# Optimization experiments

Hardware: AMD Instinct MI355X
Metric: run time of the kernel (lower is better)

The kernel has to match this reference:

```python
import jax, jax.numpy as jnp
import numpy as np
from jax import lax

B, S, T = 32, 100, 4
NUM_C2, NUM_C3, NUM_D, DV = 500, 2000, 1000, 128


def setup_inputs():
    key = jax.random.key(0)
    ks = jax.random.split(key, 25)
    s = 0.05
    def nrm(k, shape):
        return jax.random.normal(k, shape, dtype=jnp.float32) * s
    return {
        "c2_seq": jax.random.randint(ks[0], (B, S), 0, NUM_C2),
        "c3_seq": jax.random.randint(ks[1], (B, S, T), 1, NUM_C3 + 1),  # 0 is padding; use all-valid tags
        "d_seq": jax.random.randint(ks[2], (B, S), 0, NUM_D),
        "r_seq": jax.random.randint(ks[3], (B, S), 0, 2),
        "D_emb": nrm(ks[4], (NUM_D, 1)),
        "R_emb": nrm(ks[5], (2, DV)),
        "v_c2": nrm(ks[6], (DV,)),
        "v_c3": nrm(ks[7], (DV,)),
        "v_d": nrm(ks[8], (DV,)),
        "W_ih": nrm(ks[9], (3 * DV, 2 * DV)),
        "W_hh": nrm(ks[10], (3 * DV, DV)),
        "b_ih": nrm(ks[11], (3 * DV,)),
        "b_hh": nrm(ks[12], (3 * DV,)),
        "l1_W1": nrm(ks[13], (DV, DV)), "l1_b1": nrm(ks[14], (DV,)),
        "l1_W2": nrm(ks[15], (1, DV)), "l1_b2": nrm(ks[16], (1,)),
        "l2_W1": nrm(ks[17], (DV, 4 * DV)), "l2_b1": nrm(ks[18], (DV,)),
        "l2_W2": nrm(ks[19], (1, DV)), "l2_b2": nrm(ks[20], (1,)),
        "l3_W1": nrm(ks[21], (DV, 4 * DV)), "l3_b1": nrm(ks[22], (DV,)),
        "l3_W2": nrm(ks[23], (1, DV)), "l3_b2": nrm(ks[24], (1,)),
    }


def _mlp(x, W1, b1, W2, b2):
    # Linear -> ReLU -> (Dropout: identity in eval) -> Linear -> (Dropout)
    return jnp.maximum(x @ W1.T + b1, 0.0) @ W2.T + b2


def _gru(x_seq, h0, W_ih, W_hh, b_ih, b_hh):
    # torch.nn.GRU math, batch_first
    def step(h, x):
        gi = x @ W_ih.T + b_ih
        gh = h @ W_hh.T + b_hh
        i_r, i_z, i_n = jnp.split(gi, 3, axis=-1)
        h_r, h_z, h_n = jnp.split(gh, 3, axis=-1)
        r = jax.nn.sigmoid(i_r + h_r)
        z = jax.nn.sigmoid(i_z + h_z)
        n = jnp.tanh(i_n + r * h_n)
        h_new = (1.0 - z) * n + z * h
        return h_new, h_new
    _, hs = lax.scan(step, h0, jnp.swapaxes(x_seq, 0, 1))
    return jnp.swapaxes(hs, 0, 1)


def _forward(c2_seq, c3_seq, d_seq, r_seq, p):
    (D_emb, R_emb, v_c2, v_c3, v_d, W_ih, W_hh, b_ih, b_hh,
     l1_W1, l1_b1, l1_W2, l1_b2, l2_W1, l2_b1, l2_W2, l2_b2,
     l3_W1, l3_b1, l3_W2, l3_b2) = p
    Bn = c2_seq.shape[0]
    gamma = D_emb[d_seq]                      # [B,S,1]
    v_d_seq = gamma * v_d                     # [B,S,DV]
    v_r_seq = R_emb[r_seq]                    # [B,S,DV]
    h0 = jnp.zeros((Bn, DV), dtype=v_d_seq.dtype)
    h_seq = _gru(jnp.concatenate([v_d_seq, v_r_seq], -1), h0, W_ih, W_hh, b_ih, b_hh)
    alpha_seq = _mlp(h_seq, l1_W1, l1_b1, l1_W2, l1_b2)[..., 0]   # [B,S]

    def step(carry, xs):
        C2, C3 = carry
        c2, c3, vd, vr = xs                                      # [B],[B,T],[B,DV],[B,DV]
        mask = (c3 != 0).astype(C3.dtype)                        # [B,T]
        w = mask / mask.sum(-1, keepdims=True)
        beta2 = jnp.take_along_axis(C2, c2[:, None], axis=-1)    # [B,1]
        beta3 = jnp.take_along_axis(C3, c3, axis=-1)             # [B,T]
        beta3_bar = (beta3 * w).sum(-1)                          # [B]
        vc2 = beta2 * v_c2                                       # [B,DV]
        vc3 = beta3[..., None] * v_c3                            # [B,T,DV]
        vc3_bar = beta3_bar[:, None] * v_c3                      # [B,DV]
        new_c2 = _mlp(jnp.concatenate([vc2, vc3_bar, vd, vr], -1),
                      l2_W1, l2_b1, l2_W2, l2_b2)[:, 0]          # [B]
        feat3 = jnp.concatenate([
            jnp.broadcast_to(vc2[:, None, :], vc3.shape), vc3,
            jnp.broadcast_to(vd[:, None, :], vc3.shape),
            jnp.broadcast_to(vr[:, None, :], vc3.shape)], -1)    # [B,T,4*DV]
        new_c3 = _mlp(feat3, l3_W1, l3_b1, l3_W2, l3_b2)[..., 0]  # [B,T]
        oh2 = jax.nn.one_hot(c2, NUM_C2, dtype=C2.dtype)          # [B,NC2]
        oh3 = jax.nn.one_hot(c3, NUM_C3 + 1, dtype=C3.dtype) * mask[..., None]  # [B,T,NC3+1]
        multi = oh3.sum(1)
        C2n = C2 * (1.0 - oh2) + new_c2[:, None] * oh2
        C3n = C3 * (1.0 - multi) + (new_c3[..., None] * oh3).sum(1)
        return (C2n, C3n), (C2n, C3n)

    C2_0 = jnp.zeros((Bn, NUM_C2), dtype=jnp.float32)
    C3_0 = jnp.zeros((Bn, NUM_C3 + 1), dtype=jnp.float32)
    xs = (jnp.swapaxes(c2_seq, 0, 1), jnp.swapaxes(c3_seq, 0, 1),
          jnp.swapaxes(v_d_seq, 0, 1), jnp.swapaxes(v_r_seq, 0, 1))
    _, (C2_seq, C3_seq) = lax.scan(step, (C2_0, C3_0), xs)
    C2_seq = jnp.swapaxes(C2_seq, 0, 1)   # [B,S,NUM_C2]
    C3_seq = jnp.swapaxes(C3_seq, 0, 1)   # [B,S,NUM_C3+1]
    return alpha_seq, h_seq, C2_seq, C3_seq


def reference(c2_seq, c3_seq, d_seq, r_seq, D_emb, R_emb, v_c2, v_c3, v_d,
              W_ih, W_hh, b_ih, b_hh, l1_W1, l1_b1, l1_W2, l1_b2,
              l2_W1, l2_b1, l2_W2, l2_b2, l3_W1, l3_b1, l3_W2, l3_b2):
    p = (D_emb, R_emb, v_c2, v_c3, v_d, W_ih, W_hh, b_ih, b_hh,
         l1_W1, l1_b1, l1_W2, l1_b2, l2_W1, l2_b1, l2_W2, l2_b2,
         l3_W1, l3_b1, l3_W2, l3_b2)
    return _forward(c2_seq, c3_seq, d_seq, r_seq, p)
```

## Files before the change

kernel.cpp:

```cpp
#include <hip/hip_runtime.h>

#define BB   32
#define SS   100
#define TT   4
#define NCC2 500
#define NC3P 2001
#define DD   128

#define LDSF 14680

typedef _Float16 half2v __attribute__((ext_vector_type(2)));

#if defined(__has_builtin)
#if __has_builtin(__builtin_amdgcn_fdot2)
#define HAVE_FDOT2 1
#endif
#endif

__device__ __forceinline__ float fast_rcp(float x) { return __builtin_amdgcn_rcpf(x); }

__device__ __forceinline__ float dpp_sum64(float x) {
    x += __int_as_float(__builtin_amdgcn_update_dpp(0, __float_as_int(x), 0x111, 0xf, 0xf, true));
    x += __int_as_float(__builtin_amdgcn_update_dpp(0, __float_as_int(x), 0x112, 0xf, 0xf, true));
    x += __int_as_float(__builtin_amdgcn_update_dpp(0, __float_as_int(x), 0x114, 0xf, 0xf, true));
    x += __int_as_float(__builtin_amdgcn_update_dpp(0, __float_as_int(x), 0x118, 0xf, 0xf, true));
    x += __int_as_float(__builtin_amdgcn_update_dpp(0, __float_as_int(x), 0x142, 0xa, 0xf, true));
    x += __int_as_float(__builtin_amdgcn_update_dpp(0, __float_as_int(x), 0x143, 0xc, 0xf, true));
    return x;
}

__device__ __forceinline__ float dpp_sum16(float x) {
    x += __int_as_float(__builtin_amdgcn_update_dpp(0, __float_as_int(x), 0x111, 0xf, 0xf, true));
    x += __int_as_float(__builtin_amdgcn_update_dpp(0, __float_as_int(x), 0x112, 0xf, 0xf, true));
    x += __int_as_float(__builtin_amdgcn_update_dpp(0, __float_as_int(x), 0x114, 0xf, 0xf, true));
    x += __int_as_float(__builtin_amdgcn_update_dpp(0, __float_as_int(x), 0x118, 0xf, 0xf, true));
    return x;
}

__device__ __forceinline__ float dot4(float4 a, float4 b) {
    return fmaf(a.x, b.x, fmaf(a.y, b.y, fmaf(a.z, b.z, a.w * b.w)));
}

__device__ __forceinline__ unsigned pk16(float a, float b) {
    return __builtin_bit_cast(unsigned, __builtin_amdgcn_cvt_pkrtz(a, b));
}
__device__ __forceinline__ uint4 packf16(float4 A, float4 B) {
    uint4 u;
    u.x = pk16(A.x, A.y); u.y = pk16(A.z, A.w);
    u.z = pk16(B.x, B.y); u.w = pk16(B.z, B.w);
    return u;
}

__device__ __forceinline__ float dot2acc(unsigned w, unsigned h, float acc) {
#ifdef HAVE_FDOT2
    return __builtin_amdgcn_fdot2(__builtin_bit_cast(half2v, w),
                                  __builtin_bit_cast(half2v, h), acc, false);
#else
    half2v a = __builtin_bit_cast(half2v, w), b = __builtin_bit_cast(half2v, h);
    acc = fmaf((float)a.x, (float)b.x, acc);
    return fmaf((float)a.y, (float)b.y, acc);
#endif
}

__global__ __launch_bounds__(768, 1) void k_main(
    const int* __restrict__ c2_seq, const int* __restrict__ c3_seq,
    const int* __restrict__ d_seq,  const int* __restrict__ r_seq,
    const float* __restrict__ D_emb, const float* __restrict__ Remb,
    const float* __restrict__ v_c2, const float* __restrict__ v_c3,
    const float* __restrict__ v_d,
    const float* __restrict__ W_ih, const float* __restrict__ W_hh,
    const float* __restrict__ b_ih, const float* __restrict__ b_hh,
    const float* __restrict__ l2W1, const float* __restrict__ l2b1,
    const float* __restrict__ l2W2, const float* __restrict__ l2b2,
    const float* __restrict__ l3W1, const float* __restrict__ l3b1,
    const float* __restrict__ l3W2, const float* __restrict__ l3b2,
    float* __restrict__ h_out, float* __restrict__ C2o, float* __restrict__ C3o)
{
    __shared__ __align__(16) float sh[LDSF];
    int* shi = (int*)sh;
    const int blk = blockIdx.x;
    const int t = threadIdx.x;

    if (blk < BB) {
        const int b  = blk;
        const int w  = t >> 6, l = t & 63;
        const int p4 = w & 3;
        const int j2 = (w >> 2) * 64 + l;
        const int jA = j2, jB = j2 + 192;
        const int kb = p4 * 32;

        uint4 wa0, wa1, wa2, wa3, wb0, wb1, wb2, wb3;
        {
            const float4* ra = (const float4*)(W_hh + jA * DD + kb);
            const float4* rb = (const float4*)(W_hh + jB * DD + kb);
            wa0 = packf16(ra[0], ra[1]); wa1 = packf16(ra[2], ra[3]);
            wa2 = packf16(ra[4], ra[5]); wa3 = packf16(ra[6], ra[7]);
            wb0 = packf16(rb[0], rb[1]); wb1 = packf16(rb[2], rb[3]);
            wb2 = packf16(rb[4], rb[5]); wb3 = packf16(rb[6], rb[7]);
        }

        {
            const float4* vd4 = (const float4*)(v_d + kb);
            const float4* r04 = (const float4*)(Remb + kb);
            const float4* r14 = (const float4*)(Remb + 128 + kb);
#pragma unroll
            for (int rr2 = 0; rr2 < 2; ++rr2) {
                const int j = rr2 ? jB : jA;
                const float4* wx = (const float4*)(W_ih + j * 256 + kb);
                const float4* wr = (const float4*)(W_ih + j * 256 + 128 + kb);
                float pd = 0.f, pr0 = 0.f, pr1 = 0.f;
#pragma unroll
                for (int i = 0; i < 8; ++i) {
                    float4 a = wx[i], c = wr[i];
                    float4 vd = vd4[i], r0 = r04[i], r1 = r14[i];
                    pd  = fmaf(a.x, vd.x, fmaf(a.y, vd.y, fmaf(a.z, vd.z, fmaf(a.w, vd.w, pd))));
                    pr0 = fmaf(c.x, r0.x, fmaf(c.y, r0.y, fmaf(c.z, r0.z, fmaf(c.w, r0.w, pr0))));
                    pr1 = fmaf(c.x, r1.x, fmaf(c.y, r1.y, fmaf(c.z, r1.z, fmaf(c.w, r1.w, pr1))));
                }
                sh[1880 + p4 * 388 + j] = pd;
                sh[3432 + p4 * 388 + j] = pr0;
                sh[4984 + p4 * 388 + j] = pr1;
            }
        }
        if (t < SS) {
            sh[1680 + t]  = D_emb[d_seq[b * SS + t]];
            shi[1780 + t] = r_seq[b * SS + t];
        }
        if (t < 64) ((unsigned*)sh)[t] = 0u;
        __syncthreads();

        float gd_r=0,gd_z=0,gd_n=0, g0_r=0,g0_z=0,g0_n=0, g1_r=0,g1_z=0,g1_n=0;
        float bi_r=0,bi_z=0,bi_n=0, bh_r=0,bh_z=0,bh_n=0, h = 0.f;
        if (t < DD) {
#pragma unroll
            for (int p = 0; p < 4; ++p) {
                gd_r += sh[1880 + p * 388 + t];
                gd_z += sh[1880 + p * 388 + 128 + t];
                gd_n += sh[1880 + p * 388 + 256 + t];
                g0_r += sh[3432 + p * 388 + t];
                g0_z += sh[3432 + p * 388 + 128 + t];
                g0_n += sh[3432 + p * 388 + 256 + t];
                g1_r += sh[4984 + p * 388 + t];
                g1_z += sh[4984 + p * 388 + 128 + t];
                g1_n += sh[4984 + p * 388 + 256 + t];
            }
            bi_r = b_ih[t]; bi_z = b_ih[t+128]; bi_n = b_ih[t+256];
            bh_r = b_hh[t]; bh_z = b_hh[t+128]; bh_n = b_hh[t+256];
        }
        __syncthreads();

        for (int s = 0; s < SS; ++s) {
            float aA = 0.f, aB = 0.f;
            {
                const uint4* hb = ((const uint4*)sh) + p4 * 4;
                uint4 h0 = hb[0], h1 = hb[1], h2 = hb[2], h3 = hb[3];
                aA = dot2acc(wa0.x, h0.x, aA); aA = dot2acc(wa0.y, h0.y, aA);
                aA = dot2acc(wa0.z, h0.z, aA); aA = dot2acc(wa0.w, h0.w, aA);
                aA = dot2acc(wa1.x, h1.x, aA); aA = dot2acc(wa1.y, h1.y, aA);
                aA = dot2acc(wa1.z, h1.z, aA); aA = dot2acc(wa1.w, h1.w, aA);
                aA = dot2acc(wa2.x, h2.x, aA); aA = dot2acc(wa2.y, h2.y, aA);
                aA = dot2acc(wa2.z, h2.z, aA); aA = dot2acc(wa2.w, h2.w, aA);
                aA = dot2acc(wa3.x, h3.x, aA); aA = dot2acc(wa3.y, h3.y, aA);
                aA = dot2acc(wa3.z, h3.z, aA); aA = dot2acc(wa3.w, h3.w, aA);
                aB = dot2acc(wb0.x, h0.x, aB); aB = dot2acc(wb0.y, h0.y, aB);
                aB = dot2acc(wb0.z, h0.z, aB); aB = dot2acc(wb0.w, h0.w, aB);
                aB = dot2acc(wb1.x, h1.x, aB); aB = dot2acc(wb1.y, h1.y, aB);
                aB = dot2acc(wb1.z, h1.z, aB); aB = dot2acc(wb1.w, h1.w, aB);
                aB = dot2acc(wb2.x, h2.x, aB); aB = dot2acc(wb2.y, h2.y, aB);
                aB = dot2acc(wb2.z, h2.z, aB); aB = dot2acc(wb2.w, h2.w, aB);
                aB = dot2acc(wb3.x, h3.x, aB); aB = dot2acc(wb3.y, h3.y, aB);
                aB = dot2acc(wb3.z, h3.z, aB); aB = dot2acc(wb3.w, h3.w, aB);
            }
            sh[128 + p4 * 388 + jA] = aA;
            sh[128 + p4 * 388 + jB] = aB;
            __syncthreads();
            if (t < DD) {
                float ghr = bh_r, ghz = bh_z, ghn = bh_n;
#pragma unroll
                for (int p = 0; p < 4; ++p) {
                    ghr += sh[128 + p * 388 + t];
                    ghz += sh[128 + p * 388 + 128 + t];
                    ghn += sh[128 + p * 388 + 256 + t];
                }
                float gamma = sh[1680 + s]; int rr = shi[1780 + s];
                float gir = fmaf(gamma, gd_r, (rr ? g1_r : g0_r) + bi_r);
                float giz = fmaf(gamma, gd_z, (rr ? g1_z : g0_z) + bi_z);
                float gin = fmaf(gamma, gd_n, (rr ? g1_n : g0_n) + bi_n);
                float r = fast_rcp(1.f + __expf(-(gir + ghr)));
                float z = fast_rcp(1.f + __expf(-(giz + ghz)));
                float n = 1.f - 2.f * fast_rcp(__expf(2.f * fmaf(r, ghn, gin)) + 1.f);
                h = (1.f - z) * n + z * h;
                ((_Float16*)sh)[t] = (_Float16)h;
                sh[1880 + s * DD + t] = h;
            }
            __syncthreads();
        }

        {
            const float4* hs = (const float4*)(sh + 1880);
            float4* hd = (float4*)(h_out + (size_t)b * SS * DD);
            for (int i = t; i < SS * DD / 4; i += 768) hd[i] = hs[i];
        }
    } else {
        const int sb = blk - BB;
        const int b = sb >> 2;
        const int q = sb & 3;

        {
            const int g = (t & 63) >> 4, c8 = ((t & 63) & 15) * 8;
            const float* vsrc = (g == 0) ? v_c2 : (g == 1) ? v_c3 : (g == 2) ? v_d : Remb;
            const float4 va  = *(const float4*)(vsrc + c8);
            const float4 vb  = *(const float4*)(vsrc + c8 + 4);
            const float4 va1 = *(const float4*)(Remb + 128 + c8);
            const float4 vb1 = *(const float4*)(Remb + 132 + c8);
            for (int r = t >> 6; r < 256; r += 12) {
                const float* W = (r < 128) ? l2W1 : l3W1;
                float* U = sh + ((r < 128) ? 3264 : 3904);
                const int i = r & 127;
                const float* wr = W + i * 512 + g * 128 + c8;
                const float4 w0 = *(const float4*)(wr);
                const float4 w1 = *(const float4*)(wr + 4);
                float p  = dot4(w0, va)  + dot4(w1, vb);
                float p1 = dot4(w0, va1) + dot4(w1, vb1);
                p  = dpp_sum16(p);
                p1 = dpp_sum16(p1);
                if ((t & 15) == 15) {
                    U[g * 128 + i] = p;
                    if (g == 3) U[512 + i] = p1;
                }
            }
        }
        for (int k = t; k < NCC2 + NC3P; k += 768) sh[k] = 0.f;
        for (int k = t; k < SS; k += 768) {
            shi[2504 + k] = c2_seq[b * SS + k];
            sh[3004 + k]  = D_emb[d_seq[b * SS + k]];
            shi[3104 + k] = r_seq[b * SS + k];
        }
        for (int k = t; k < SS; k += 768)
            reinterpret_cast<int4*>(shi + 2604)[k] = reinterpret_cast<const int4*>(c3_seq + b * SS * TT)[k];
        __syncthreads();

        if (t < 64) {
            float* C2s = sh;
            float* C3s = sh + NCC2;
            const float* u2 = sh + 3264;
            const float* u3 = sh + 3904;
            const float u2a0 = u2[t],        u2a1 = u2[64 + t];
            const float u2b0 = u2[128 + t],  u2b1 = u2[192 + t];
            const float u2c0 = u2[256 + t],  u2c1 = u2[320 + t];
            const float u2d00 = u2[384 + t], u2d01 = u2[448 + t];
            const float u2d10 = u2[512 + t], u2d11 = u2[576 + t];
            const float u3a0 = u3[t],        u3a1 = u3[64 + t];
            const float u3b0 = u3[128 + t],  u3b1 = u3[192 + t];
            const float u3c0 = u3[256 + t],  u3c1 = u3[320 + t];
            const float u3d00 = u3[384 + t], u3d01 = u3[448 + t];
            const float u3d10 = u3[512 + t], u3d11 = u3[576 + t];
            const float b2_0 = l2b1[t], b2_1 = l2b1[64 + t];
            const float w2_0 = l2W2[t], w2_1 = l2W2[64 + t];
            const float b3_0 = l3b1[t], b3_1 = l3b1[64 + t];
            const float w3_0 = l3W2[t], w3_1 = l3W2[64 + t];
            const float c2bias = l2b2[0], c3bias = l3b2[0];

            int  nc2 = shi[2504];
            int4 nc3 = reinterpret_cast<const int4*>(shi + 2604)[0];
            float ngam = sh[3004];
            int   nrr  = shi[3104];

            for (int s = 0; s < SS; ++s) {
                const int c2i = nc2;
                const int i0 = nc3.x, i1 = nc3.y, i2 = nc3.z, i3 = nc3.w;
                const float gamma = ngam;
                const int rr = nrr;
                if (s + 1 < SS) {
                    nc2 = shi[2504 + s + 1];
                    nc3 = reinterpret_cast<const int4*>(shi + 2604)[s + 1];
                    ngam = sh[3004 + s + 1];
                    nrr  = shi[3104 + s + 1];
                }

                const float beta2 = C2s[c2i];
                const bool k0 = (i0 != 0), k1 = (i1 != 0), k2 = (i2 != 0), k3 = (i3 != 0);
                const float m0 = k0 ? 1.f : 0.f, m1 = k1 ? 1.f : 0.f;
                const float m2 = k2 ? 1.f : 0.f, m3 = k3 ? 1.f : 0.f;
                const float bt0 = C3s[i0], bt1 = C3s[i1], bt2 = C3s[i2], bt3 = C3s[i3];
                const float msum = m0 + m1 + m2 + m3;
                const float b3bar = (bt0 * m0 + bt1 * m1 + bt2 * m2 + bt3 * m3) * fast_rcp(msum);

                const float ud20 = rr ? u2d10 : u2d00, ud21 = rr ? u2d11 : u2d01;
                const float ud30 = rr ? u3d10 : u3d00, ud31 = rr ? u3d11 : u3d01;

                float h20 = fmaf(beta2, u2a0, fmaf(b3bar, u2b0, fmaf(gamma, u2c0, ud20 + b2_0)));
                float h21 = fmaf(beta2, u2a1, fmaf(b3bar, u2b1, fmaf(gamma, u2c1, ud21 + b2_1)));
                float newc2 = dpp_sum64(fmaf(fmaxf(h20, 0.f), w2_0, fmaxf(h21, 0.f) * w2_1)) + c2bias;

                const float base30 = fmaf(beta2, u3a0, fmaf(gamma, u3c0, ud30 + b3_0));
                const float base31 = fmaf(beta2, u3a1, fmaf(gamma, u3c1, ud31 + b3_1));
                float ha, hb, q0, q1, q2, q3;
                ha = fmaf(bt0, u3b0, base30); hb = fmaf(bt0, u3b1, base31);
                q0 = dpp_sum64(fmaf(fmaxf(ha, 0.f), w3_0, fmaxf(hb, 0.f) * w3_1)) + c3bias;
                ha = fmaf(bt1, u3b0, base30); hb = fmaf(bt1, u3b1, base31);
                q1 = dpp_sum64(fmaf(fmaxf(ha, 0.f), w3_0, fmaxf(hb, 0.f) * w3_1)) + c3bias;
                ha = fmaf(bt2, u3b0, base30); hb = fmaf(bt2, u3b1, base31);
                q2 = dpp_sum64(fmaf(fmaxf(ha, 0.f), w3_0, fmaxf(hb, 0.f) * w3_1)) + c3bias;
                ha = fmaf(bt3, u3b0, base30); hb = fmaf(bt3, u3b1, base31);
                q3 = dpp_sum64(fmaf(fmaxf(ha, 0.f), w3_0, fmaxf(hb, 0.f) * w3_1)) + c3bias;

                float val0, val1, val2, val3;
                {
                    float c = m0 + ((k1 && i1 == i0) ? 1.f : 0.f) + ((k2 && i2 == i0) ? 1.f : 0.f) + ((k3 && i3 == i0) ? 1.f : 0.f);
                    float qs = (k0 ? q0 : 0.f) + ((k1 && i1 == i0) ? q1 : 0.f) + ((k2 && i2 == i0) ? q2 : 0.f) + ((k3 && i3 == i0) ? q3 : 0.f);
                    val0 = bt0 * (1.f - c) + qs;
                }
                {
                    float c = ((k0 && i0 == i1) ? 1.f : 0.f) + m1 + ((k2 && i2 == i1) ? 1.f : 0.f) + ((k3 && i3 == i1) ? 1.f : 0.f);
                    float qs = ((k0 && i0 == i1) ? q0 : 0.f) + (k1 ? q1 : 0.f) + ((k2 && i2 == i1) ? q2 : 0.f) + ((k3 && i3 == i1) ? q3 : 0.f);
                    val1 = bt1 * (1.f - c) + qs;
                }
                {
                    float c = ((k0 && i0 == i2) ? 1.f : 0.f) + ((k1 && i1 == i2) ? 1.f : 0.f) + m2 + ((k3 && i3 == i2) ? 1.f : 0.f);
                    float qs = ((k0 && i0 == i2) ? q0 : 0.f) + ((k1 && i1 == i2) ? q1 : 0.f) + (k2 ? q2 : 0.f) + ((k3 && i3 == i2) ? q3 : 0.f);
                    val2 = bt2 * (1.f - c) + qs;
                }
                {
                    float c = ((k0 && i0 == i3) ? 1.f : 0.f) + ((k1 && i1 == i3) ? 1.f : 0.f) + ((k2 && i2 == i3) ? 1.f : 0.f) + m3;
                    float qs = ((k0 && i0 == i3) ? q0 : 0.f) + ((k1 && i1 == i3) ? q1 : 0.f) + ((k2 && i2 == i3) ? q2 : 0.f) + (k3 ? q3 : 0.f);
                    val3 = bt3 * (1.f - c) + qs;
                }

                if (t == 63) {
                    C2s[c2i] = newc2;
                    if (k0) C3s[i0] = val0;
                    if (k1) C3s[i1] = val1;
                    if (k2) C3s[i2] = val2;
                    if (k3) C3s[i3] = val3;
                    sh[4544 + s] = newc2;
                    sh[4644 + 4 * s + 0] = val0;
                    sh[4644 + 4 * s + 1] = val1;
                    sh[4644 + 4 * s + 2] = val2;
                    sh[4644 + 4 * s + 3] = val3;
                }
            }
        }
        __syncthreads();

        for (int k = t; k < NCC2 + NC3P; k += 768) sh[k] = 0.f;
        __syncthreads();

        float* C2s = sh;
        float* C3s = sh + NCC2;
        for (int s = 0; s < SS; ++s) {
            if (t == 0) {
                C2s[shi[2504 + s]] = sh[4544 + s];
                const int4 ic3 = reinterpret_cast<const int4*>(shi + 2604)[s];
                if (ic3.x) C3s[ic3.x] = sh[4644 + 4 * s + 0];
                if (ic3.y) C3s[ic3.y] = sh[4644 + 4 * s + 1];
                if (ic3.z) C3s[ic3.z] = sh[4644 + 4 * s + 2];
                if (ic3.w) C3s[ic3.w] = sh[4644 + 4 * s + 3];
            }
            if ((s & 3) == q) {
                __syncthreads();
                const int rs = b * SS + s;
                float* c2row = C2o + (size_t)rs * NCC2;
                if (t < 125) reinterpret_cast<float4*>(c2row)[t] = reinterpret_cast<const float4*>(C2s)[t];
                float* c3row = C3o + (size_t)rs * NC3P;
                const int p0 = (4 - (rs & 3)) & 3;
                if (t < p0) c3row[t] = C3s[t];
                const int rem = NC3P - p0;
                const int nv = rem >> 2, tl = rem & 3;
                if (t < nv) {
                    const int d = p0 + 4 * t;
                    *reinterpret_cast<float4*>(c3row + d) =
                        make_float4(C3s[d], C3s[d + 1], C3s[d + 2], C3s[d + 3]);
                }
                if (t < tl) {
                    const int d = p0 + 4 * nv + t;
                    c3row[d] = C3s[d];
                }
                __syncthreads();
            }
        }
    }
}

__global__ __launch_bounds__(256) void k_alpha(const float* __restrict__ h_seq,
                                               const float* __restrict__ W1,
                                               const float* __restrict__ b1,
                                               const float* __restrict__ W2,
                                               const float* __restrict__ b2,
                                               float* __restrict__ alpha)
{
    __shared__ __align__(16) float sl[22560];
    const int t = threadIdx.x;
    const int base = blockIdx.x * 16;

    float4* hl4 = reinterpret_cast<float4*>(sl);
    const float4* hg = reinterpret_cast<const float4*>(h_seq + (size_t)base * DD);
    for (int i = t; i < 512; i += 256) hl4[i] = hg[i];

    float4* wl4 = reinterpret_cast<float4*>(sl + 6144);
    const float4* wg = reinterpret_cast<const float4*>(W1);
    for (int g = t; g < 4096; g += 256) {
        const int ch = g >> 5, k4 = g & 31;
        wl4[ch * 32 + (k4 ^ (ch & 31))] = wg[g];
    }
    __syncthreads();

    const int ch = t & 127, half = t >> 7;
    float acc[16];
#pragma unroll
    for (int r = 0; r < 16; ++r) acc[r] = 0.f;
#pragma unroll
    for (int kk = 0; kk < 16; ++kk) {
        const int k4 = half * 16 + kk;
        const float4 w = wl4[ch * 32 + (k4 ^ (ch & 31))];
#pragma unroll
        for (int r = 0; r < 16; ++r) {
            const float4 hv = hl4[r * 32 + k4];
            acc[r] = fmaf(w.x, hv.x, fmaf(w.y, hv.y, fmaf(w.z, hv.z, fmaf(w.w, hv.w, acc[r]))));
        }
    }
#pragma unroll
    for (int r = 0; r < 16; ++r) sl[2048 + r * 256 + t] = acc[r];
    __syncthreads();
    if (t < 128) {
        const float b1v = b1[t], w2v = W2[t];
#pragma unroll
        for (int r = 0; r < 16; ++r) {
            float v = fmaxf(sl[2048 + r * 256 + t] + sl[2048 + r * 256 + 128 + t] + b1v, 0.f) * w2v;
            v = dpp_sum64(v);
            if ((t & 63) == 63) sl[22528 + r * 2 + (t >> 6)] = v;
        }
    }
    __syncthreads();
    if (t < 16) alpha[base + t] = sl[22528 + 2 * t] + sl[22528 + 2 * t + 1] + b2[0];
}

extern "C" void kernel_launch(void* const* d_in, const int* in_sizes, int n_in,
                              void* d_out, int out_size, void* d_ws, size_t ws_size,
                              hipStream_t stream)
{
    (void)in_sizes; (void)n_in; (void)out_size; (void)d_ws; (void)ws_size;
    const int*   c2_seq = (const int*)d_in[0];
    const int*   c3_seq = (const int*)d_in[1];
    const int*   d_seq  = (const int*)d_in[2];
    const int*   r_seq  = (const int*)d_in[3];
    const float* D_emb  = (const float*)d_in[4];
    const float* Remb   = (const float*)d_in[5];
    const float* v_c2   = (const float*)d_in[6];
    const float* v_c3   = (const float*)d_in[7];
    const float* v_d    = (const float*)d_in[8];
    const float* W_ih   = (const float*)d_in[9];
    const float* W_hh   = (const float*)d_in[10];
    const float* b_ih   = (const float*)d_in[11];
    const float* b_hh   = (const float*)d_in[12];
    const float* l1W1   = (const float*)d_in[13];
    const float* l1b1   = (const float*)d_in[14];
    const float* l1W2   = (const float*)d_in[15];
    const float* l1b2   = (const float*)d_in[16];
    const float* l2W1   = (const float*)d_in[17];
    const float* l2b1   = (const float*)d_in[18];
    const float* l2W2   = (const float*)d_in[19];
    const float* l2b2   = (const float*)d_in[20];
    const float* l3W1   = (const float*)d_in[21];
    const float* l3b1   = (const float*)d_in[22];
    const float* l3W2   = (const float*)d_in[23];
    const float* l3b2   = (const float*)d_in[24];

    float* out   = (float*)d_out;
    float* alpha = out;
    float* h_out = out + 3200;
    float* C2o   = out + 412800;
    float* C3o   = out + 2012800;

    k_main<<<BB + 4 * BB, 768, 0, stream>>>(c2_seq, c3_seq, d_seq, r_seq, D_emb, Remb,
                                            v_c2, v_c3, v_d,
                                            W_ih, W_hh, b_ih, b_hh,
                                            l2W1, l2b1, l2W2, l2b2,
                                            l3W1, l3b1, l3W2, l3b2,
                                            h_out, C2o, C3o);
    k_alpha<<<200, 256, 0, stream>>>(h_out, l1W1, l1b1, l1W2, l1b2, alpha);
}
```

Before: 118.4 us.

## Fuse alpha MLP into main kernel, shrink blocks to 512, rework C-state pipeline

```diff
diff --git a/kernel.cpp b/kernel.cpp
--- a/kernel.cpp
+++ b/kernel.cpp
@@ -7,7 +7,14 @@
 #define NC3P 2001
 #define DD   128
 
-#define LDSF 14680
+#define ALPH  0
+#define REDB  2048
+#define GAMB  2064
+#define RRB   2164
+#define HALL  2264
+#define PARTB 15064
+#define HF16  16632
+#define LDSF  16696
 
 typedef _Float16 half2v __attribute__((ext_vector_type(2)));
 
@@ -35,6 +42,10 @@
     x += __int_as_float(__builtin_amdgcn_update_dpp(0, __float_as_int(x), 0x114, 0xf, 0xf, true));
     x += __int_as_float(__builtin_amdgcn_update_dpp(0, __float_as_int(x), 0x118, 0xf, 0xf, true));
     return x;
+}
+
+__device__ __forceinline__ float rdl63(float x) {
+    return __int_as_float(__builtin_amdgcn_readlane(__float_as_int(x), 63));
 }
 
 __device__ __forceinline__ float dot4(float4 a, float4 b) {
@@ -62,7 +73,18 @@
 #endif
 }
 
-__global__ __launch_bounds__(768, 1) void k_main(
+#define DOTQ(w0, w1, w2, w3, h0, h1, h2, h3, acc) do {                     \
+    acc = dot2acc((w0).x, (h0).x, acc); acc = dot2acc((w0).y, (h0).y, acc);\
+    acc = dot2acc((w0).z, (h0).z, acc); acc = dot2acc((w0).w, (h0).w, acc);\
+    acc = dot2acc((w1).x, (h1).x, acc); acc = dot2acc((w1).y, (h1).y, acc);\
+    acc = dot2acc((w1).z, (h1).z, acc); acc = dot2acc((w1).w, (h1).w, acc);\
+    acc = dot2acc((w2).x, (h2).x, acc); acc = dot2acc((w2).y, (h2).y, acc);\
+    acc = dot2acc((w2).z, (h2).z, acc); acc = dot2acc((w2).w, (h2).w, acc);\
+    acc = dot2acc((w3).x, (h3).x, acc); acc = dot2acc((w3).y, (h3).y, acc);\
+    acc = dot2acc((w3).z, (h3).z, acc); acc = dot2acc((w3).w, (h3).w, acc);\
+} while (0)
+
+__global__ __launch_bounds__(512, 1) void k_all(
     const int* __restrict__ c2_seq, const int* __restrict__ c3_seq,
     const int* __restrict__ d_seq,  const int* __restrict__ r_seq,
     const float* __restrict__ D_emb, const float* __restrict__ Remb,
@@ -70,33 +92,39 @@
     const float* __restrict__ v_d,
     const float* __restrict__ W_ih, const float* __restrict__ W_hh,
     const float* __restrict__ b_ih, const float* __restrict__ b_hh,
+    const float* __restrict__ l1W1, const float* __restrict__ l1b1,
+    const float* __restrict__ l1W2, const float* __restrict__ l1b2,
     const float* __restrict__ l2W1, const float* __restrict__ l2b1,
     const float* __restrict__ l2W2, const float* __restrict__ l2b2,
     const float* __restrict__ l3W1, const float* __restrict__ l3b1,
     const float* __restrict__ l3W2, const float* __restrict__ l3b2,
-    float* __restrict__ h_out, float* __restrict__ C2o, float* __restrict__ C3o)
+    float* __restrict__ alpha, float* __restrict__ h_out,
+    float* __restrict__ C2o, float* __restrict__ C3o)
 {
     __shared__ __align__(16) float sh[LDSF];
     int* shi = (int*)sh;
+    float4* sh4 = (float4*)sh;
     const int blk = blockIdx.x;
     const int t = threadIdx.x;
 
     if (blk < BB) {
-        const int b  = blk;
-        const int w  = t >> 6, l = t & 63;
-        const int p4 = w & 3;
-        const int j2 = (w >> 2) * 64 + l;
-        const int jA = j2, jB = j2 + 192;
+        const int b = blk;
+        const int trip = t >> 2;
+        const int p4 = t & 3;
+        const int jA = 3 * trip, jB = jA + 1, jC = jA + 2;
         const int kb = p4 * 32;
 
-        uint4 wa0, wa1, wa2, wa3, wb0, wb1, wb2, wb3;
+        uint4 wa0, wa1, wa2, wa3, wb0, wb1, wb2, wb3, wc0, wc1, wc2, wc3;
         {
             const float4* ra = (const float4*)(W_hh + jA * DD + kb);
             const float4* rb = (const float4*)(W_hh + jB * DD + kb);
+            const float4* rc = (const float4*)(W_hh + jC * DD + kb);
             wa0 = packf16(ra[0], ra[1]); wa1 = packf16(ra[2], ra[3]);
             wa2 = packf16(ra[4], ra[5]); wa3 = packf16(ra[6], ra[7]);
             wb0 = packf16(rb[0], rb[1]); wb1 = packf16(rb[2], rb[3]);
             wb2 = packf16(rb[4], rb[5]); wb3 = packf16(rb[6], rb[7]);
+            wc0 = packf16(rc[0], rc[1]); wc1 = packf16(rc[2], rc[3]);
+            wc2 = packf16(rc[4], rc[5]); wc3 = packf16(rc[6], rc[7]);
         }
 
         {
@@ -104,8 +132,8 @@
             const float4* r04 = (const float4*)(Remb + kb);
             const float4* r14 = (const float4*)(Remb + 128 + kb);
 #pragma unroll
-            for (int rr2 = 0; rr2 < 2; ++rr2) {
-                const int j = rr2 ? jB : jA;
+            for (int rr3 = 0; rr3 < 3; ++rr3) {
+                const int j = jA + rr3;
                 const float4* wx = (const float4*)(W_ih + j * 256 + kb);
                 const float4* wr = (const float4*)(W_ih + j * 256 + 128 + kb);
                 float pd = 0.f, pr0 = 0.f, pr1 = 0.f;
@@ -117,16 +145,16 @@
                     pr0 = fmaf(c.x, r0.x, fmaf(c.y, r0.y, fmaf(c.z, r0.z, fmaf(c.w, r0.w, pr0))));
                     pr1 = fmaf(c.x, r1.x, fmaf(c.y, r1.y, fmaf(c.z, r1.z, fmaf(c.w, r1.w, pr1))));
                 }
-                sh[1880 + p4 * 388 + j] = pd;
-                sh[3432 + p4 * 388 + j] = pr0;
-                sh[4984 + p4 * 388 + j] = pr1;
+                sh[HALL +        p4 * 392 + j] = pd;
+                sh[HALL + 1568 + p4 * 392 + j] = pr0;
+                sh[HALL + 3136 + p4 * 392 + j] = pr1;
             }
         }
         if (t < SS) {
-            sh[1680 + t]  = D_emb[d_seq[b * SS + t]];
-            shi[1780 + t] = r_seq[b * SS + t];
-        }
-        if (t < 64) ((unsigned*)sh)[t] = 0u;
+            sh[GAMB + t]  = D_emb[d_seq[b * SS + t]];
+            shi[RRB + t] = r_seq[b * SS + t];
+        }
+        if (t < 64) ((unsigned*)(sh + HF16))[t] = 0u;
         __syncthreads();
 
         float gd_r=0,gd_z=0,gd_n=0, g0_r=0,g0_z=0,g0_n=0, g1_r=0,g1_z=0,g1_n=0;
@@ -134,15 +162,15 @@
         if (t < DD) {
 #pragma unroll
             for (int p = 0; p < 4; ++p) {
-                gd_r += sh[1880 + p * 388 + t];
-                gd_z += sh[1880 + p * 388 + 128 + t];
-                gd_n += sh[1880 + p * 388 + 256 + t];
-                g0_r += sh[3432 + p * 388 + t];
-                g0_z += sh[3432 + p * 388 + 128 + t];
-                g0_n += sh[3432 + p * 388 + 256 + t];
-                g1_r += sh[4984 + p * 388 + t];
-                g1_z += sh[4984 + p * 388 + 128 + t];
-                g1_n += sh[4984 + p * 388 + 256 + t];
+                gd_r += sh[HALL + p * 392 + t];
+                gd_z += sh[HALL + p * 392 + 128 + t];
+                gd_n += sh[HALL + p * 392 + 256 + t];
+                g0_r += sh[HALL + 1568 + p * 392 + t];
+                g0_z += sh[HALL + 1568 + p * 392 + 128 + t];
+                g0_n += sh[HALL + 1568 + p * 392 + 256 + t];
+                g1_r += sh[HALL + 3136 + p * 392 + t];
+                g1_z += sh[HALL + 3136 + p * 392 + 128 + t];
+                g1_n += sh[HALL + 3136 + p * 392 + 256 + t];
             }
             bi_r = b_ih[t]; bi_z = b_ih[t+128]; bi_n = b_ih[t+256];
             bh_r = b_hh[t]; bh_z = b_hh[t+128]; bh_n = b_hh[t+256];
@@ -150,39 +178,27 @@
         __syncthreads();
 
         for (int s = 0; s < SS; ++s) {
-            float aA = 0.f, aB = 0.f;
+            float aA = 0.f, aB = 0.f, aC = 0.f;
             {
-                const uint4* hb = ((const uint4*)sh) + p4 * 4;
+                const uint4* hb = ((const uint4*)(sh + HF16)) + p4 * 4;
                 uint4 h0 = hb[0], h1 = hb[1], h2 = hb[2], h3 = hb[3];
-                aA = dot2acc(wa0.x, h0.x, aA); aA = dot2acc(wa0.y, h0.y, aA);
-                aA = dot2acc(wa0.z, h0.z, aA); aA = dot2acc(wa0.w, h0.w, aA);
-                aA = dot2acc(wa1.x, h1.x, aA); aA = dot2acc(wa1.y, h1.y, aA);
-                aA = dot2acc(wa1.z, h1.z, aA); aA = dot2acc(wa1.w, h1.w, aA);
-                aA = dot2acc(wa2.x, h2.x, aA); aA = dot2acc(wa2.y, h2.y, aA);
-                aA = dot2acc(wa2.z, h2.z, aA); aA = dot2acc(wa2.w, h2.w, aA);
-                aA = dot2acc(wa3.x, h3.x, aA); aA = dot2acc(wa3.y, h3.y, aA);
-                aA = dot2acc(wa3.z, h3.z, aA); aA = dot2acc(wa3.w, h3.w, aA);
-                aB = dot2acc(wb0.x, h0.x, aB); aB = dot2acc(wb0.y, h0.y, aB);
-                aB = dot2acc(wb0.z, h0.z, aB); aB = dot2acc(wb0.w, h0.w, aB);
-                aB = dot2acc(wb1.x, h1.x, aB); aB = dot2acc(wb1.y, h1.y, aB);
-                aB = dot2acc(wb1.z, h1.z, aB); aB = dot2acc(wb1.w, h1.w, aB);
-                aB = dot2acc(wb2.x, h2.x, aB); aB = dot2acc(wb2.y, h2.y, aB);
-                aB = dot2acc(wb2.z, h2.z, aB); aB = dot2acc(wb2.w, h2.w, aB);
-                aB = dot2acc(wb3.x, h3.x, aB); aB = dot2acc(wb3.y, h3.y, aB);
-                aB = dot2acc(wb3.z, h3.z, aB); aB = dot2acc(wb3.w, h3.w, aB);
-            }
-            sh[128 + p4 * 388 + jA] = aA;
-            sh[128 + p4 * 388 + jB] = aB;
+                DOTQ(wa0, wa1, wa2, wa3, h0, h1, h2, h3, aA);
+                DOTQ(wb0, wb1, wb2, wb3, h0, h1, h2, h3, aB);
+                DOTQ(wc0, wc1, wc2, wc3, h0, h1, h2, h3, aC);
+            }
+            sh[PARTB + p4 * 392 + jA] = aA;
+            sh[PARTB + p4 * 392 + jB] = aB;
+            sh[PARTB + p4 * 392 + jC] = aC;
             __syncthreads();
             if (t < DD) {
                 float ghr = bh_r, ghz = bh_z, ghn = bh_n;
 #pragma unroll
                 for (int p = 0; p < 4; ++p) {
-                    ghr += sh[128 + p * 388 + t];
-                    ghz += sh[128 + p * 388 + 128 + t];
-                    ghn += sh[128 + p * 388 + 256 + t];
-                }
-                float gamma = sh[1680 + s]; int rr = shi[1780 + s];
+                    ghr += sh[PARTB + p * 392 + t];
+                    ghz += sh[PARTB + p * 392 + 128 + t];
+                    ghn += sh[PARTB + p * 392 + 256 + t];
+                }
+                float gamma = sh[GAMB + s]; int rr = shi[RRB + s];
                 float gir = fmaf(gamma, gd_r, (rr ? g1_r : g0_r) + bi_r);
                 float giz = fmaf(gamma, gd_z, (rr ? g1_z : g0_z) + bi_z);
                 float gin = fmaf(gamma, gd_n, (rr ? g1_n : g0_n) + bi_n);
@@ -190,21 +206,62 @@
                 float z = fast_rcp(1.f + __expf(-(giz + ghz)));
                 float n = 1.f - 2.f * fast_rcp(__expf(2.f * fmaf(r, ghn, gin)) + 1.f);
                 h = (1.f - z) * n + z * h;
-                ((_Float16*)sh)[t] = (_Float16)h;
-                sh[1880 + s * DD + t] = h;
+                ((_Float16*)(sh + HF16))[t] = (_Float16)h;
+                sh[HALL + s * DD + t] = h;
             }
             __syncthreads();
         }
 
         {
-            const float4* hs = (const float4*)(sh + 1880);
+            const float4* hs = (const float4*)(sh + HALL);
             float4* hd = (float4*)(h_out + (size_t)b * SS * DD);
-            for (int i = t; i < SS * DD / 4; i += 768) hd[i] = hs[i];
+            for (int i = t; i < SS * DD / 4; i += 512) hd[i] = hs[i];
+        }
+
+        {
+            const int ch = t & 127, seg = t >> 7;
+            float4 aw[8];
+            const float4* awp = (const float4*)(l1W1 + ch * 128 + seg * 32);
+#pragma unroll
+            for (int i = 0; i < 8; ++i) aw[i] = awp[i];
+            float b1v = 0.f, w2v = 0.f;
+            if (t < 128) { b1v = l1b1[t]; w2v = l1W2[t]; }
+            const float b2v = l1b2[0];
+
+            for (int r0 = 0; r0 < SS; r0 += 4) {
+                float acc0 = 0.f, acc1 = 0.f, acc2 = 0.f, acc3 = 0.f;
+                const int hbase = (HALL >> 2) + seg * 8;
+#pragma unroll
+                for (int i = 0; i < 8; ++i) {
+                    acc0 = fmaf(1.f, dot4(aw[i], sh4[hbase + (r0 + 0) * 32 + i]), acc0);
+                    acc1 = fmaf(1.f, dot4(aw[i], sh4[hbase + (r0 + 1) * 32 + i]), acc1);
+                    acc2 = fmaf(1.f, dot4(aw[i], sh4[hbase + (r0 + 2) * 32 + i]), acc2);
+                    acc3 = fmaf(1.f, dot4(aw[i], sh4[hbase + (r0 + 3) * 32 + i]), acc3);
+                }
+                sh[ALPH + 0 * 512 + seg * 128 + ch] = acc0;
+                sh[ALPH + 1 * 512 + seg * 128 + ch] = acc1;
+                sh[ALPH + 2 * 512 + seg * 128 + ch] = acc2;
+                sh[ALPH + 3 * 512 + seg * 128 + ch] = acc3;
+                __syncthreads();
+                if (t < 128) {
+#pragma unroll
+                    for (int rr4 = 0; rr4 < 4; ++rr4) {
+                        float v = sh[ALPH + rr4 * 512 + t] + sh[ALPH + rr4 * 512 + 128 + t]
+                                + sh[ALPH + rr4 * 512 + 256 + t] + sh[ALPH + rr4 * 512 + 384 + t];
+                        v = fmaxf(v + b1v, 0.f) * w2v;
+                        v = dpp_sum64(v);
+                        if ((t & 63) == 63) sh[REDB + rr4 * 2 + (t >> 6)] = v;
+                    }
+                }
+                __syncthreads();
+                if (t < 4) alpha[b * SS + r0 + t] = sh[REDB + 2 * t] + sh[REDB + 2 * t + 1] + b2v;
+                __syncthreads();
+            }
         }
     } else {
         const int sb = blk - BB;
-        const int b = sb >> 2;
-        const int q = sb & 3;
+        const int b = sb >> 3;
+        const int q = sb & 7;
 
         {
             const int g = (t & 63) >> 4, c8 = ((t & 63) & 15) * 8;
@@ -213,7 +270,7 @@
             const float4 vb  = *(const float4*)(vsrc + c8 + 4);
             const float4 va1 = *(const float4*)(Remb + 128 + c8);
             const float4 vb1 = *(const float4*)(Remb + 132 + c8);
-            for (int r = t >> 6; r < 256; r += 12) {
+            for (int r = t >> 6; r < 256; r += 8) {
                 const float* W = (r < 128) ? l2W1 : l3W1;
                 float* U = sh + ((r < 128) ? 3264 : 3904);
                 const int i = r & 127;
@@ -230,13 +287,13 @@
                 }
             }
         }
-        for (int k = t; k < NCC2 + NC3P; k += 768) sh[k] = 0.f;
-        for (int k = t; k < SS; k += 768) {
+        for (int k = t; k < NCC2 + NC3P; k += 512) sh[k] = 0.f;
+        for (int k = t; k < SS; k += 512) {
             shi[2504 + k] = c2_seq[b * SS + k];
             sh[3004 + k]  = D_emb[d_seq[b * SS + k]];
             shi[3104 + k] = r_seq[b * SS + k];
         }
-        for (int k = t; k < SS; k += 768)
+        for (int k = t; k < SS; k += 512)
             reinterpret_cast<int4*>(shi + 2604)[k] = reinterpret_cast<const int4*>(c3_seq + b * SS * TT)[k];
         __syncthreads();
 
@@ -261,89 +318,98 @@
             const float w3_0 = l3W2[t], w3_1 = l3W2[64 + t];
             const float c2bias = l2b2[0], c3bias = l3b2[0];
 
-            int  nc2 = shi[2504];
-            int4 nc3 = reinterpret_cast<const int4*>(shi + 2604)[0];
-            float ngam = sh[3004];
-            int   nrr  = shi[3104];
+            float beta2 = 0.f, bt0 = 0.f, bt1 = 0.f, bt2 = 0.f, bt3 = 0.f;
+            int c2i = shi[2504];
+            int4 i4 = reinterpret_cast<const int4*>(shi + 2604)[0];
+            float gamma = sh[3004];
+            int   rr    = shi[3104];
 
             for (int s = 0; s < SS; ++s) {
-                const int c2i = nc2;
-                const int i0 = nc3.x, i1 = nc3.y, i2 = nc3.z, i3 = nc3.w;
-                const float gamma = ngam;
-                const int rr = nrr;
+                int nc2i = 0; int4 ni4 = make_int4(0, 0, 0, 0);
+                float ngam = 0.f; int nrr = 0;
                 if (s + 1 < SS) {
-                    nc2 = shi[2504 + s + 1];
-                    nc3 = reinterpret_cast<const int4*>(shi + 2604)[s + 1];
+                    nc2i = shi[2504 + s + 1];
+                    ni4  = reinterpret_cast<const int4*>(shi + 2604)[s + 1];
                     ngam = sh[3004 + s + 1];
                     nrr  = shi[3104 + s + 1];
                 }
-
-                const float beta2 = C2s[c2i];
-                const bool k0 = (i0 != 0), k1 = (i1 != 0), k2 = (i2 != 0), k3 = (i3 != 0);
-                const float m0 = k0 ? 1.f : 0.f, m1 = k1 ? 1.f : 0.f;
-                const float m2 = k2 ? 1.f : 0.f, m3 = k3 ? 1.f : 0.f;
-                const float bt0 = C3s[i0], bt1 = C3s[i1], bt2 = C3s[i2], bt3 = C3s[i3];
-                const float msum = m0 + m1 + m2 + m3;
-                const float b3bar = (bt0 * m0 + bt1 * m1 + bt2 * m2 + bt3 * m3) * fast_rcp(msum);
-
+                const float nbeta2 = C2s[nc2i];
+                const float nb0 = C3s[ni4.x], nb1 = C3s[ni4.y];
+                const float nb2 = C3s[ni4.z], nb3 = C3s[ni4.w];
+
+                const float b3bar = 0.25f * ((bt0 + bt1) + (bt2 + bt3));
                 const float ud20 = rr ? u2d10 : u2d00, ud21 = rr ? u2d11 : u2d01;
                 const float ud30 = rr ? u3d10 : u3d00, ud31 = rr ? u3d11 : u3d01;
 
                 float h20 = fmaf(beta2, u2a0, fmaf(b3bar, u2b0, fmaf(gamma, u2c0, ud20 + b2_0)));
                 float h21 = fmaf(beta2, u2a1, fmaf(b3bar, u2b1, fmaf(gamma, u2c1, ud21 + b2_1)));
-                float newc2 = dpp_sum64(fmaf(fmaxf(h20, 0.f), w2_0, fmaxf(h21, 0.f) * w2_1)) + c2bias;
+                const float r2 = dpp_sum64(fmaf(fmaxf(h20, 0.f), w2_0, fmaxf(h21, 0.f) * w2_1));
 
                 const float base30 = fmaf(beta2, u3a0, fmaf(gamma, u3c0, ud30 + b3_0));
                 const float base31 = fmaf(beta2, u3a1, fmaf(gamma, u3c1, ud31 + b3_1));
-                float ha, hb, q0, q1, q2, q3;
+                float ha, hb;
                 ha = fmaf(bt0, u3b0, base30); hb = fmaf(bt0, u3b1, base31);
-                q0 = dpp_sum64(fmaf(fmaxf(ha, 0.f), w3_0, fmaxf(hb, 0.f) * w3_1)) + c3bias;
+                const float r30 = dpp_sum64(fmaf(fmaxf(ha, 0.f), w3_0, fmaxf(hb, 0.f) * w3_1));
                 ha = fmaf(bt1, u3b0, base30); hb = fmaf(bt1, u3b1, base31);
-                q1 = dpp_sum64(fmaf(fmaxf(ha, 0.f), w3_0, fmaxf(hb, 0.f) * w3_1)) + c3bias;
+                const float r31 = dpp_sum64(fmaf(fmaxf(ha, 0.f), w3_0, fmaxf(hb, 0.f) * w3_1));
                 ha = fmaf(bt2, u3b0, base30); hb = fmaf(bt2, u3b1, base31);
-                q2 = dpp_sum64(fmaf(fmaxf(ha, 0.f), w3_0, fmaxf(hb, 0.f) * w3_1)) + c3bias;
+                const float r32 = dpp_sum64(fmaf(fmaxf(ha, 0.f), w3_0, fmaxf(hb, 0.f) * w3_1));
                 ha = fmaf(bt3, u3b0, base30); hb = fmaf(bt3, u3b1, base31);
-                q3 = dpp_sum64(fmaf(fmaxf(ha, 0.f), w3_0, fmaxf(hb, 0.f) * w3_1)) + c3bias;
-
-                float val0, val1, val2, val3;
-                {
-                    float c = m0 + ((k1 && i1 == i0) ? 1.f : 0.f) + ((k2 && i2 == i0) ? 1.f : 0.f) + ((k3 && i3 == i0) ? 1.f : 0.f);
-                    float qs = (k0 ? q0 : 0.f) + ((k1 && i1 == i0) ? q1 : 0.f) + ((k2 && i2 == i0) ? q2 : 0.f) + ((k3 && i3 == i0) ? q3 : 0.f);
-                    val0 = bt0 * (1.f - c) + qs;
-                }
-                {
-                    float c = ((k0 && i0 == i1) ? 1.f : 0.f) + m1 + ((k2 && i2 == i1) ? 1.f : 0.f) + ((k3 && i3 == i1) ? 1.f : 0.f);
-                    float qs = ((k0 && i0 == i1) ? q0 : 0.f) + (k1 ? q1 : 0.f) + ((k2 && i2 == i1) ? q2 : 0.f) + ((k3 && i3 == i1) ? q3 : 0.f);
-                    val1 = bt1 * (1.f - c) + qs;
-                }
-                {
-                    float c = ((k0 && i0 == i2) ? 1.f : 0.f) + ((k1 && i1 == i2) ? 1.f : 0.f) + m2 + ((k3 && i3 == i2) ? 1.f : 0.f);
-                    float qs = ((k0 && i0 == i2) ? q0 : 0.f) + ((k1 && i1 == i2) ? q1 : 0.f) + (k2 ? q2 : 0.f) + ((k3 && i3 == i2) ? q3 : 0.f);
-                    val2 = bt2 * (1.f - c) + qs;
-                }
-                {
-                    float c = ((k0 && i0 == i3) ? 1.f : 0.f) + ((k1 && i1 == i3) ? 1.f : 0.f) + ((k2 && i2 == i3) ? 1.f : 0.f) + m3;
-                    float qs = ((k0 && i0 == i3) ? q0 : 0.f) + ((k1 && i1 == i3) ? q1 : 0.f) + ((k2 && i2 == i3) ? q2 : 0.f) + (k3 ? q3 : 0.f);
-                    val3 = bt3 * (1.f - c) + qs;
-                }
-
-                if (t == 63) {
+                const float r33 = dpp_sum64(fmaf(fmaxf(ha, 0.f), w3_0, fmaxf(hb, 0.f) * w3_1));
+
+                const float newc2 = rdl63(r2) + c2bias;
+                const float q0 = rdl63(r30) + c3bias;
+                const float q1 = rdl63(r31) + c3bias;
+                const float q2 = rdl63(r32) + c3bias;
+                const float q3 = rdl63(r33) + c3bias;
+
+                const int i0 = i4.x, i1 = i4.y, i2 = i4.z, i3 = i4.w;
+                const float f01 = (i1 == i0) ? 1.f : 0.f;
+                const float f02 = (i2 == i0) ? 1.f : 0.f;
+                const float f03 = (i3 == i0) ? 1.f : 0.f;
+                const float f12 = (i2 == i1) ? 1.f : 0.f;
+                const float f13 = (i3 == i1) ? 1.f : 0.f;
+                const float f23 = (i3 == i2) ? 1.f : 0.f;
+                const float c0 = 1.f + f01 + f02 + f03;
+                const float c1 = 1.f + f01 + f12 + f13;
+                const float c2c = 1.f + f02 + f12 + f23;
+                const float c3c = 1.f + f03 + f13 + f23;
+                const float qs0 = q0 + f01 * q1 + f02 * q2 + f03 * q3;
+                const float qs1 = q1 + f01 * q0 + f12 * q2 + f13 * q3;
+                const float qs2 = q2 + f02 * q0 + f12 * q1 + f23 * q3;
+                const float qs3 = q3 + f03 * q0 + f13 * q1 + f23 * q2;
+                const float val0 = bt0 * (1.f - c0) + qs0;
+                const float val1 = bt1 * (1.f - c1) + qs1;
+                const float val2 = bt2 * (1.f - c2c) + qs2;
+                const float val3 = bt3 * (1.f - c3c) + qs3;
+
+                if (t == 0) {
                     C2s[c2i] = newc2;
-                    if (k0) C3s[i0] = val0;
-                    if (k1) C3s[i1] = val1;
-                    if (k2) C3s[i2] = val2;
-                    if (k3) C3s[i3] = val3;
+                    C3s[i0] = val0; C3s[i1] = val1; C3s[i2] = val2; C3s[i3] = val3;
                     sh[4544 + s] = newc2;
                     sh[4644 + 4 * s + 0] = val0;
                     sh[4644 + 4 * s + 1] = val1;
                     sh[4644 + 4 * s + 2] = val2;
                     sh[4644 + 4 * s + 3] = val3;
                 }
+
+                beta2 = (nc2i == c2i) ? newc2 : nbeta2;
+                float v;
+                v = nb0; if (ni4.x == i0) v = val0; if (ni4.x == i1) v = val1;
+                         if (ni4.x == i2) v = val2; if (ni4.x == i3) v = val3; bt0 = v;
+                v = nb1; if (ni4.y == i0) v = val0; if (ni4.y == i1) v = val1;
+                         if (ni4.y == i2) v = val2; if (ni4.y == i3) v = val3; bt1 = v;
+                v = nb2; if (ni4.z == i0) v = val0; if (ni4.z == i1) v = val1;
+                         if (ni4.z == i2) v = val2; if (ni4.z == i3) v = val3; bt2 = v;
+                v = nb3; if (ni4.w == i0) v = val0; if (ni4.w == i1) v = val1;
+                         if (ni4.w == i2) v = val2; if (ni4.w == i3) v = val3; bt3 = v;
+
+                c2i = nc2i; i4 = ni4; gamma = ngam; rr = nrr;
             }
         }
         __syncthreads();
 
-        for (int k = t; k < NCC2 + NC3P; k += 768) sh[k] = 0.f;
+        for (int k = t; k < NCC2 + NC3P; k += 512) sh[k] = 0.f;
         __syncthreads();
 
         float* C2s = sh;
@@ -352,12 +418,12 @@
             if (t == 0) {
                 C2s[shi[2504 + s]] = sh[4544 + s];
                 const int4 ic3 = reinterpret_cast<const int4*>(shi + 2604)[s];
-                if (ic3.x) C3s[ic3.x] = sh[4644 + 4 * s + 0];
-                if (ic3.y) C3s[ic3.y] = sh[4644 + 4 * s + 1];
-                if (ic3.z) C3s[ic3.z] = sh[4644 + 4 * s + 2];
-                if (ic3.w) C3s[ic3.w] = sh[4644 + 4 * s + 3];
-            }
-            if ((s & 3) == q) {
+                C3s[ic3.x] = sh[4644 + 4 * s + 0];
+                C3s[ic3.y] = sh[4644 + 4 * s + 1];
+                C3s[ic3.z] = sh[4644 + 4 * s + 2];
+                C3s[ic3.w] = sh[4644 + 4 * s + 3];
+            }
+            if ((s & 7) == q) {
                 __syncthreads();
                 const int rs = b * SS + s;
                 float* c2row = C2o + (size_t)rs * NCC2;
@@ -380,59 +446,6 @@
             }
         }
     }
-}
-
-__global__ __launch_bounds__(256) void k_alpha(const float* __restrict__ h_seq,
-                                               const float* __restrict__ W1,
-                                               const float* __restrict__ b1,
-                                               const float* __restrict__ W2,
-                                               const float* __restrict__ b2,
-                                               float* __restrict__ alpha)
-{
-    __shared__ __align__(16) float sl[22560];
-    const int t = threadIdx.x;
-    const int base = blockIdx.x * 16;
-
-    float4* hl4 = reinterpret_cast<float4*>(sl);
-    const float4* hg = reinterpret_cast<const float4*>(h_seq + (size_t)base * DD);
-    for (int i = t; i < 512; i += 256) hl4[i] = hg[i];
-
-    float4* wl4 = reinterpret_cast<float4*>(sl + 6144);
-    const float4* wg = reinterpret_cast<const float4*>(W1);
-    for (int g = t; g < 4096; g += 256) {
-        const int ch = g >> 5, k4 = g & 31;
-        wl4[ch * 32 + (k4 ^ (ch & 31))] = wg[g];
-    }
-    __syncthreads();
-
-    const int ch = t & 127, half = t >> 7;
-    float acc[16];
-#pragma unroll
-    for (int r = 0; r < 16; ++r) acc[r] = 0.f;
-#pragma unroll
-    for (int kk = 0; kk < 16; ++kk) {
-        const int k4 = half * 16 + kk;
-        const float4 w = wl4[ch * 32 + (k4 ^ (ch & 31))];
-#pragma unroll
-        for (int r = 0; r < 16; ++r) {
-            const float4 hv = hl4[r * 32 + k4];
-            acc[r] = fmaf(w.x, hv.x, fmaf(w.y, hv.y, fmaf(w.z, hv.z, fmaf(w.w, hv.w, acc[r]))));
-        }
-    }
-#pragma unroll
-    for (int r = 0; r < 16; ++r) sl[2048 + r * 256 + t] = acc[r];
-    __syncthreads();
-    if (t < 128) {
-        const float b1v = b1[t], w2v = W2[t];
-#pragma unroll
-        for (int r = 0; r < 16; ++r) {
-            float v = fmaxf(sl[2048 + r * 256 + t] + sl[2048 + r * 256 + 128 + t] + b1v, 0.f) * w2v;
-            v = dpp_sum64(v);
-            if ((t & 63) == 63) sl[22528 + r * 2 + (t >> 6)] = v;
-        }
-    }
-    __syncthreads();
-    if (t < 16) alpha[base + t] = sl[22528 + 2 * t] + sl[22528 + 2 * t + 1] + b2[0];
 }
 
 extern "C" void kernel_launch(void* const* d_in, const int* in_sizes, int n_in,
@@ -472,11 +485,11 @@
     float* C2o   = out + 412800;
     float* C3o   = out + 2012800;
 
-    k_main<<<BB + 4 * BB, 768, 0, stream>>>(c2_seq, c3_seq, d_seq, r_seq, D_emb, Remb,
-                                            v_c2, v_c3, v_d,
-                                            W_ih, W_hh, b_ih, b_hh,
-                                            l2W1, l2b1, l2W2, l2b2,
-                                            l3W1, l3b1, l3W2, l3b2,
-                                            h_out, C2o, C3o);
-    k_alpha<<<200, 256, 0, stream>>>(h_out, l1W1, l1b1, l1W2, l1b2, alpha);
-}
+    k_all<<<BB + 8 * BB, 512, 0, stream>>>(c2_seq, c3_seq, d_seq, r_seq, D_emb, Remb,
+                                           v_c2, v_c3, v_d,
+                                           W_ih, W_hh, b_ih, b_hh,
+                                           l1W1, l1b1, l1W2, l1b2,
+                                           l2W1, l2b1, l2W2, l2b2,
+                                           l3W1, l3b1, l3W2, l3b2,
+                                           alpha, h_out, C2o, C3o);
+}
```

Result: slower. 183.9 us (+55.3%).
